# Kernel optimization log

Measured on AMD Instinct MI355X. Metric: run time of the kernel, lower is better.

The kernel has to match this reference:

```python
import jax, jax.numpy as jnp
import numpy as np

GROUPS = 64; SIDE = 8; STEPS = 8
TAU = 1.0; FLOOR = 1e-4; EPS = 1e-4
MU = 1.0; DT = 0.1; GAMMA = 0.1
FLOW_W = 1.0; LOCAL_W = 0.5; KEEP_RATIO = 0.5


def _with_floor(m):
    n = m.shape[-1]
    mask = 1.0 - jnp.eye(n, dtype=m.dtype)
    return jnp.maximum(m * mask, FLOOR * mask)


def _norm_scores(s):
    mean = s.mean(axis=1, keepdims=True)
    std = jnp.clip(s.std(axis=1, ddof=1, keepdims=True), 1e-6, None)  # torch unbiased std
    return (s - mean) / std


def _router_core(tokens, cls_token, W, grid_h, grid_w):
    B, P, D = tokens.shape
    # group ids from patch grid position (patch_indices defaults to arange)
    pi = jnp.broadcast_to(jnp.arange(P), (B, P))
    row, col = pi // grid_w, pi % grid_w
    gh = -(-grid_h // SIDE); gw = -(-grid_w // SIDE)  # ceil div
    gid = jnp.minimum(row // gh, SIDE - 1) * SIDE + jnp.minimum(col // gw, SIDE - 1)  # [B,P]
    # mean-pool tokens per group (scatter_add + count)
    seg = jax.vmap(lambda t, g: jax.ops.segment_sum(t, g, num_segments=GROUPS))
    grouped = seg(tokens, gid)                                 # [B,G,D]
    counts = seg(jnp.ones((B, P, 1), tokens.dtype), gid)       # [B,G,1]
    grouped = grouped / jnp.maximum(counts, 1.0)
    nodes = jnp.concatenate([cls_token[:, None, :], grouped], axis=1)  # [B,G+1,D]
    # pairwise conductance: project, l2-normalize, squared cdist, exp kernel
    proj = jnp.einsum('bnd,ed->bne', nodes, W)  # Linear (no bias): x @ W.T
    proj = proj / jnp.maximum(jnp.linalg.norm(proj, axis=-1, keepdims=True), 1e-12)
    sq = jnp.sum(proj * proj, axis=-1)
    d2 = jnp.maximum(sq[:, :, None] + sq[:, None, :]
                     - 2.0 * jnp.einsum('bnd,bmd->bnm', proj, proj), 0.0)
    C = _with_floor(jnp.exp(-d2 / TAU))
    C = 0.5 * (C + jnp.swapaxes(C, -1, -2))  # symmetric
    # source: cls node injects, groups drain
    source = jnp.full((B, GROUPS + 1), -1.0 / GROUPS, C.dtype).at[:, 0].set(1.0)
    N = GROUPS + 1
    I = jnp.eye(N, dtype=C.dtype)
    d_list, q_list = [C], []
    for _ in range(STEPS):
        deg = C.sum(-1)
        system = deg[:, :, None] * I - C + EPS * I            # Laplacian + eps*I
        p = jnp.linalg.solve(system, source[..., None])[..., 0]
        flow = C * (p[:, :, None] - p[:, None, :])
        q_list.append(flow)
        r = jnp.abs(flow) ** MU
        r = r / (1.0 + r)
        C = C + DT * (r - GAMMA * C)
        C = _with_floor(jnp.maximum(C, 0.0))
        C = _with_floor(0.5 * (C + jnp.swapaxes(C, -1, -2)))
        d_list.append(C)
    return C, jnp.stack(d_list, 1), jnp.stack(q_list, 1), gid


def setup_inputs() -> dict:
    key = jax.random.key(0)
    k1, k2, k3, k4 = jax.random.split(key, 4)
    B, P, D = 64, 576, 768
    return {
        'tokens': jax.random.normal(k1, (B, P, D), jnp.float32),
        'cls_token': jax.random.normal(k2, (B, D), jnp.float32),
        'W': jax.random.normal(k3, (D, D), jnp.float32) / np.sqrt(D),
        'local_scores': jax.random.normal(k4, (B, P), jnp.float32),
        'grid_h': 24,
        'grid_w': 24,
    }


def reference(tokens, cls_token, W, local_scores, grid_h, grid_w):
    B, P, _ = tokens.shape
    final_d, d_hist, q_hist, gid = _router_core(tokens, cls_token, W, grid_h, grid_w)
    routing = final_d[:, 1:, 1:]
    routing = routing / jnp.clip(routing.sum(-1, keepdims=True), 1e-6, None)
    group_flow = jnp.abs(q_hist[:, -1, 1:, :]).sum(-1)        # [B,G]
    group_scores = jnp.take_along_axis(_norm_scores(group_flow), gid, axis=1)
    token_scores = FLOW_W * group_scores + LOCAL_W * _norm_scores(local_scores)
    keep_count = max(1, int(round(P * KEEP_RATIO)))
    _, topk = jax.lax.top_k(token_scores, keep_count)
    patch_keep_mask = jnp.zeros((B, P), bool).at[jnp.arange(B)[:, None], topk].set(True)
    keep_mask = jnp.concatenate([jnp.ones((B, 1), bool), patch_keep_mask], axis=1)
    delta = d_hist[:, 1:] - d_hist[:, :-1]
    aux_sparse = final_d[:, 1:, 1:].sum(axis=(-1, -2)).mean()
    aux_stable = jnp.abs(delta).sum(axis=(-1, -2, -3)).mean()
    return (keep_mask, patch_keep_mask, gid, group_scores, d_hist, q_hist,
            routing, aux_sparse, aux_stable)
```

## Files before the change

kernel.cpp:

```cpp
#include <hip/hip_runtime.h>
#include <stdint.h>

#define NB 64
#define NP 576
#define ND 768
#define NG 64
#define NN 65
#define NSTEPS 8
#define FLOORV 1.0e-4f
#define EPSV   1.0e-4f
#define DTV    0.1f
#define GAMMAV 0.1f
#define KEEPC  288
#define PITCH2 68

__global__ __launch_bounds__(256) void k_group_means(const float* __restrict__ tokens,
                                                     const float* __restrict__ cls,
                                                     float* __restrict__ nodes,
                                                     const int* __restrict__ ghp,
                                                     const int* __restrict__ gwp) {
    int bx = blockIdx.x;
    int b = bx / NN, n = bx - b * NN;
    int tid = threadIdx.x;
    float* orow = nodes + (size_t)bx * ND;
    if (n == 0) {
        for (int d = tid; d < ND; d += 256) orow[d] = cls[(size_t)b * ND + d];
        return;
    }
    int grid_h = *ghp, grid_w = *gwp;
    int gh = (grid_h + 7) / 8, gw = (grid_w + 7) / 8;
    int g = n - 1, gr = g >> 3, gc = g & 7;
    int r0 = gr * gh, r1 = (gr == 7) ? grid_h : min((gr + 1) * gh, grid_h);
    int c0 = gc * gw, c1 = (gc == 7) ? grid_w : min((gc + 1) * gw, grid_w);
    int cnt = (r1 > r0 && c1 > c0) ? (r1 - r0) * (c1 - c0) : 0;
    float cf = (float)max(cnt, 1);
    const float* tb = tokens + (size_t)b * NP * ND;
    for (int d = tid; d < ND; d += 256) {
        float acc = 0.f;
        for (int r = r0; r < r1; ++r)
            for (int c = c0; c < c1; ++c)
                acc += tb[(size_t)(r * grid_w + c) * ND + d];
        orow[d] = acc / cf;
    }
}

__global__ __launch_bounds__(256) void k_gemm_nt(const float* __restrict__ A,
                                                 const float* __restrict__ Bm,
                                                 float* __restrict__ Cm) {
    __shared__ float As[32][68];
    __shared__ float Bs[32][68];
    int tid = threadIdx.x;
    int m0 = blockIdx.x * 64, n0 = blockIdx.y * 64;
    int tx = tid & 15, ty = tid >> 4;
    float acc[4][4];
#pragma unroll
    for (int i = 0; i < 4; ++i)
#pragma unroll
        for (int j = 0; j < 4; ++j) acc[i][j] = 0.f;
    int lrow = tid >> 3, lq = tid & 7;
    for (int k0 = 0; k0 < ND; k0 += 32) {
#pragma unroll
        for (int l = 0; l < 2; ++l) {
            int row = lrow + l * 32;
            float4 va = *(const float4*)&A[(size_t)(m0 + row) * ND + k0 + lq * 4];
            As[lq * 4 + 0][row] = va.x; As[lq * 4 + 1][row] = va.y;
            As[lq * 4 + 2][row] = va.z; As[lq * 4 + 3][row] = va.w;
            float4 vb = *(const float4*)&Bm[(size_t)(n0 + row) * ND + k0 + lq * 4];
            Bs[lq * 4 + 0][row] = vb.x; Bs[lq * 4 + 1][row] = vb.y;
            Bs[lq * 4 + 2][row] = vb.z; Bs[lq * 4 + 3][row] = vb.w;
        }
        __syncthreads();
#pragma unroll
        for (int kk = 0; kk < 32; ++kk) {
            float4 a4 = *(const float4*)&As[kk][ty * 4];
            float4 b4 = *(const float4*)&Bs[kk][tx * 4];
            float av[4] = {a4.x, a4.y, a4.z, a4.w};
            float bv[4] = {b4.x, b4.y, b4.z, b4.w};
#pragma unroll
            for (int i = 0; i < 4; ++i)
#pragma unroll
                for (int j = 0; j < 4; ++j) acc[i][j] += av[i] * bv[j];
        }
        __syncthreads();
    }
#pragma unroll
    for (int i = 0; i < 4; ++i) {
        float4 o = make_float4(acc[i][0], acc[i][1], acc[i][2], acc[i][3]);
        *(float4*)&Cm[(size_t)(m0 + ty * 4 + i) * ND + n0 + tx * 4] = o;
    }
}

__global__ __launch_bounds__(256) void k_normalize(float* __restrict__ proj, float* __restrict__ sqv) {
    int r = blockIdx.x, tid = threadIdx.x;
    __shared__ double red[8];
    __shared__ float invs;
    float* row = proj + (size_t)r * ND;
    double s = 0.0;
    for (int d = tid; d < ND; d += 256) { double v = (double)row[d]; s += v * v; }
#pragma unroll
    for (int off = 32; off; off >>= 1) s += __shfl_down(s, off, 64);
    int wid = tid >> 6, lane = tid & 63;
    if (lane == 0) red[wid] = s;
    __syncthreads();
    if (tid == 0) invs = (float)(1.0 / fmax(sqrt(red[0] + red[1] + red[2] + red[3]), 1e-12));
    __syncthreads();
    float inv = invs;
    double s2 = 0.0;
    for (int d = tid; d < ND; d += 256) {
        float v = row[d] * inv; row[d] = v; s2 += (double)v * (double)v;
    }
#pragma unroll
    for (int off = 32; off; off >>= 1) s2 += __shfl_down(s2, off, 64);
    __syncthreads();
    if (lane == 0) red[wid] = s2;
    __syncthreads();
    if (tid == 0) sqv[r] = (float)(red[0] + red[1] + red[2] + red[3]);
}

__global__ __launch_bounds__(256) void k_pairwise(const float* __restrict__ proj,
                                                  const float* __restrict__ sqv,
                                                  float* __restrict__ dhist) {
    int b = blockIdx.x, tid = threadIdx.x;
    int tx = tid & 15, ty = tid >> 4;
    __shared__ float Ps[NN][65];
    float acc[5][5];
#pragma unroll
    for (int a = 0; a < 5; ++a)
#pragma unroll
        for (int c = 0; c < 5; ++c) acc[a][c] = 0.f;
    const float* Pb = proj + (size_t)b * NN * ND;
    for (int k0 = 0; k0 < ND; k0 += 64) {
        __syncthreads();
        for (int idx = tid; idx < NN * 64; idx += 256) {
            int i = idx >> 6, kk = idx & 63;
            Ps[i][kk] = Pb[(size_t)i * ND + k0 + kk];
        }
        __syncthreads();
        for (int kk = 0; kk < 64; ++kk) {
            float av[5], bv[5];
#pragma unroll
            for (int a = 0; a < 5; ++a) { int i = ty + 16 * a; av[a] = (i < NN) ? Ps[i][kk] : 0.f; }
#pragma unroll
            for (int c = 0; c < 5; ++c) { int j = tx + 16 * c; bv[c] = (j < NN) ? Ps[j][kk] : 0.f; }
#pragma unroll
            for (int a = 0; a < 5; ++a)
#pragma unroll
                for (int c = 0; c < 5; ++c) acc[a][c] += av[a] * bv[c];
        }
    }
#pragma unroll
    for (int a = 0; a < 5; ++a)
#pragma unroll
        for (int c = 0; c < 5; ++c) {
            int i = ty + 16 * a, j = tx + 16 * c;
            if (i < NN && j < NN) {
                float d2 = fmaxf(sqv[b * NN + i] + sqv[b * NN + j] - 2.0f * acc[a][c], 0.f);
                double cv = exp(-(double)d2);
                float cf = (i == j) ? 0.f : fmaxf((float)cv, FLOORV);
                dhist[(size_t)b * 9 * NN * NN + (size_t)i * NN + j] = cf;
            }
        }
}

__global__ __launch_bounds__(256) void k_dynamics(float* __restrict__ dhist,
                                                  float* __restrict__ qhist,
                                                  double* __restrict__ part) {
    int b = blockIdx.x, tid = threadIdx.x;
    __shared__ float Cs[NN * NN];
    __shared__ float Aug[NN * PITCH2];
    __shared__ float pd[NN];
    __shared__ double redd[8];
    float* C0 = dhist + (size_t)b * 9 * NN * NN;
    for (int t = tid; t < NN * NN; t += 256) Cs[t] = C0[t];
    __syncthreads();

    int r = tid >> 2, q = tid & 3;
    const int my_i = r + 1;
    float* mrow = Aug + my_i * PITCH2;
    double stable = 0.0, sparse = 0.0;

#pragma unroll 1
    for (int step = 0; step < NSTEPS; ++step) {
        for (int t = tid; t < NN * PITCH2; t += 256) {
            int i = t / PITCH2, j = t - i * PITCH2;
            if (j != i && j != NN)
                Aug[t] = (j < NN) ? -Cs[i * NN + j] : 0.f;
        }
        if (tid < NN) {
            float s = 0.f;
            const float* cr = Cs + tid * NN;
#pragma unroll 4
            for (int j = 0; j < NN; ++j) s += cr[j];
            Aug[tid * PITCH2 + tid] = s + EPSV;
            Aug[tid * PITCH2 + NN] = (tid == 0) ? 1.0f : (-1.0f / NG);
        }
        __syncthreads();

#pragma unroll 1
        for (int k = 0; k < NN - 1; k += 2) {
            if (my_i > k + 1) {
                const float* P = Aug + k * PITCH2;
                const float* Q = P + PITCH2;
                float Pk = P[k], Pk1 = P[k + 1];
                float Qk = Q[k], Qk1 = Q[k + 1];
                float Aik = mrow[k], Aik1 = mrow[k + 1];
                float invP = 1.0f / Pk;
                float h = Qk * invP;
                float Qd = Qk1 - h * Pk1;
                float f = Aik * invP;
                float g = (Aik1 - f * Pk1) / Qd;
                float c1 = f - g * h, c2 = g;
                const float4* P4 = (const float4*)P;
                const float4* Q4 = (const float4*)Q;
                float4* M4 = (float4*)mrow;
#pragma unroll
                for (int u = 0; u < 4; ++u) {
                    int t = q + 4 * u;
                    float4 p = P4[t], qv = Q4[t], m = M4[t];
                    m.x -= c1 * p.x + c2 * qv.x;
                    m.y -= c1 * p.y + c2 * qv.y;
                    m.z -= c1 * p.z + c2 * qv.z;
                    m.w -= c1 * p.w + c2 * qv.w;
                    M4[t] = m;
                }
                if (q == 0) {
                    float4 p = P4[16], qv = Q4[16], m = M4[16];
                    m.x -= c1 * p.x + c2 * qv.x;
                    m.y -= c1 * p.y + c2 * qv.y;
                    m.z -= c1 * p.z + c2 * qv.z;
                    m.w -= c1 * p.w + c2 * qv.w;
                    M4[16] = m;
                }
            }
            __syncthreads();
        }

        {
            int fr = 2 * (tid >> 3) + 1;
            int l8 = tid & 7;
            float* R = Aug + fr * PITCH2;
            const float* Pp = R - PITCH2;
            float h = R[fr - 1] / Pp[fr - 1];
            float4* R4 = (float4*)R;
            const float4* Pp4 = (const float4*)Pp;
#pragma unroll
            for (int u = 0; u < 2; ++u) {
                int t = l8 + 8 * u;
                float4 a = R4[t], p = Pp4[t];
                a.x -= h * p.x; a.y -= h * p.y; a.z -= h * p.z; a.w -= h * p.w;
                R4[t] = a;
            }
            if (l8 == 0) {
                float4 a = R4[16], p = Pp4[16];
                a.x -= h * p.x; a.y -= h * p.y; a.z -= h * p.z; a.w -= h * p.w;
                R4[16] = a;
            }
        }
        __syncthreads();

        if (tid < 64) {
            int lane = tid;
            int i_own = lane + 1;
            const float* brow = Aug + i_own * PITCH2;
            float inv_own = 1.0f / brow[i_own];
            float rhs = brow[NN];
            float acc = 0.f, p_own = 0.f;
#pragma unroll 2
            for (int i = NN - 1; i >= 1; --i) {
                float t = (rhs - acc) * inv_own;
                float pi = __shfl(t, i - 1, 64);
                if (i_own == i) p_own = t;
                acc += ((lane < i - 1) ? brow[i] : 0.f) * pi;
                if (lane == 0) pd[i] = pi;
            }
            float sp0 = Cs[i_own] * p_own;
#pragma unroll
            for (int off = 32; off; off >>= 1) sp0 += __shfl_down(sp0, off, 64);
            if (lane == 0) pd[0] = (1.0f + sp0) / Aug[0];
        }
        __syncthreads();

        float* qout = qhist + ((size_t)b * NSTEPS + step) * NN * NN;
        float* dout = dhist + ((size_t)b * 9 + step + 1) * NN * NN;
        for (int t = tid; t < NN * NN; t += 256) {
            int i = t / NN, j = t - i * NN;
            float c = Cs[t];
            float fl = c * (pd[i] - pd[j]);
            qout[t] = fl;
            float rr = fabsf(fl); rr = rr / (1.0f + rr);
            float cn = c + DTV * (rr - GAMMAV * c);
            float cnf = (i == j) ? 0.0f : fmaxf(cn, FLOORV);
            Cs[t] = cnf;
            dout[t] = cnf;
            stable += fabs((double)cnf - (double)c);
            if (step == NSTEPS - 1 && i > 0 && j > 0) sparse += (double)cnf;
        }
        __syncthreads();
    }

#pragma unroll
    for (int off = 32; off; off >>= 1) {
        stable += __shfl_down(stable, off, 64);
        sparse += __shfl_down(sparse, off, 64);
    }
    int wid = tid >> 6, lane = tid & 63;
    if (lane == 0) { redd[wid] = stable; redd[4 + wid] = sparse; }
    __syncthreads();
    if (tid == 0) {
        part[b]      = redd[4] + redd[5] + redd[6] + redd[7];
        part[NB + b] = redd[0] + redd[1] + redd[2] + redd[3];
    }
}

__global__ __launch_bounds__(256) void k_scores(const float* __restrict__ qhist,
                                                const float* __restrict__ local,
                                                const int* __restrict__ ghp,
                                                const int* __restrict__ gwp,
                                                float* __restrict__ keep,
                                                float* __restrict__ patch,
                                                float* __restrict__ gidout,
                                                float* __restrict__ gsout) {
    int b = blockIdx.x, tid = threadIdx.x;
    __shared__ double gf[NG];
    __shared__ double ts[NP];
    __shared__ double red[8];
    __shared__ double stats[2];
    if (tid < NG) {
        const float* qrow = qhist + ((size_t)b * NSTEPS + (NSTEPS - 1)) * NN * NN + (size_t)(tid + 1) * NN;
        double s = 0.0;
        for (int j = 0; j < NN; ++j) s += fabs((double)qrow[j]);
        gf[tid] = s;
    }
    __syncthreads();
    if (tid < 64) {
        double v = gf[tid];
        double s = v;
#pragma unroll
        for (int off = 32; off; off >>= 1) s += __shfl_down(s, off, 64);
        double mean = __shfl(s, 0, 64) / (double)NG;
        double d = v - mean, ss = d * d;
#pragma unroll
        for (int off = 32; off; off >>= 1) ss += __shfl_down(ss, off, 64);
        if (tid == 0) { stats[0] = mean; stats[1] = 1.0 / fmax(sqrt(ss / (NG - 1)), 1e-6); }
    }
    const float* lrow = local + (size_t)b * NP;
    double s1 = 0.0;
    for (int p = tid; p < NP; p += 256) s1 += (double)lrow[p];
#pragma unroll
    for (int off = 32; off; off >>= 1) s1 += __shfl_down(s1, off, 64);
    int wid = tid >> 6, lane = tid & 63;
    if (lane == 0) red[wid] = s1;
    __syncthreads();
    double lmean = (red[0] + red[1] + red[2] + red[3]) / (double)NP;
    double s2 = 0.0;
    for (int p = tid; p < NP; p += 256) { double d = (double)lrow[p] - lmean; s2 += d * d; }
#pragma unroll
    for (int off = 32; off; off >>= 1) s2 += __shfl_down(s2, off, 64);
    __syncthreads();
    if (lane == 0) red[wid] = s2;
    __syncthreads();
    double linv = 1.0 / fmax(sqrt((red[0] + red[1] + red[2] + red[3]) / (double)(NP - 1)), 1e-6);
    double gmean = stats[0], ginv = stats[1];
    int grid_h = *ghp, grid_w = *gwp;
    int gh = (grid_h + 7) / 8, gw = (grid_w + 7) / 8;
    for (int p = tid; p < NP; p += 256) {
        int row = p / grid_w, col = p - row * grid_w;
        int g = min(row / gh, 7) * 8 + min(col / gw, 7);
        double gsc = (gf[g] - gmean) * ginv;
        double lsc = ((double)lrow[p] - lmean) * linv;
        ts[p] = gsc + 0.5 * lsc;
        gidout[(size_t)b * NP + p] = (float)g;
        gsout[(size_t)b * NP + p]  = (float)gsc;
    }
    __syncthreads();
    for (int p = tid; p < NP; p += 256) {
        double sp = ts[p];
        int c = 0;
        for (int qq = 0; qq < NP; ++qq) {
            double v = ts[qq];
            c += (v > sp) || (v == sp && qq < p);
        }
        float kf = (c < KEEPC) ? 1.0f : 0.0f;
        patch[(size_t)b * NP + p] = kf;
        keep[(size_t)b * (NP + 1) + 1 + p] = kf;
    }
    if (tid == 0) keep[(size_t)b * (NP + 1)] = 1.0f;
}

__global__ void k_routing(const float* __restrict__ dhist, float* __restrict__ rout) {
    int b = blockIdx.x, tid = threadIdx.x;
    const float* Crow = dhist + ((size_t)b * 9 + 8) * NN * NN + (size_t)(tid + 1) * NN + 1;
    double s = 0.0;
    for (int j = 0; j < NG; ++j) s += (double)Crow[j];
    double inv = 1.0 / fmax(s, 1e-6);
    float* orow = rout + ((size_t)b * NG + tid) * NG;
    for (int j = 0; j < NG; ++j) orow[j] = (float)((double)Crow[j] * inv);
}

__global__ void k_aux(const double* __restrict__ part, float* __restrict__ osp, float* __restrict__ ost) {
    int tid = threadIdx.x;
    double sp = part[tid], st = part[NB + tid];
#pragma unroll
    for (int off = 32; off; off >>= 1) {
        sp += __shfl_down(sp, off, 64);
        st += __shfl_down(st, off, 64);
    }
    if (tid == 0) { *osp = (float)(sp / NB); *ost = (float)(st / NB); }
}

extern "C" void kernel_launch(void* const* d_in, const int* in_sizes, int n_in,
                              void* d_out, int out_size, void* d_ws, size_t ws_size,
                              hipStream_t stream) {
    const float* tokens = (const float*)d_in[0];
    const float* cls    = (const float*)d_in[1];
    const float* W      = (const float*)d_in[2];
    const float* local  = (const float*)d_in[3];
    const int* ghp = (const int*)d_in[4];
    const int* gwp = (const int*)d_in[5];

    float* out = (float*)d_out;
    float* o_keep  = out;
    float* o_patch = o_keep + (size_t)NB * (NP + 1);
    float* o_gid   = o_patch + (size_t)NB * NP;
    float* o_gs    = o_gid + (size_t)NB * NP;
    float* o_dh    = o_gs + (size_t)NB * NP;
    float* o_qh    = o_dh + (size_t)NB * 9 * NN * NN;
    float* o_rt    = o_qh + (size_t)NB * NSTEPS * NN * NN;
    float* o_sp    = o_rt + (size_t)NB * NG * NG;
    float* o_st    = o_sp + 1;

    float* nodes = (float*)d_ws;
    float* proj  = nodes + (size_t)NB * NN * ND;
    float* sqv   = proj + (size_t)NB * NN * ND;
    double* part = (double*)(((uintptr_t)(sqv + NB * NN) + 15) & ~(uintptr_t)15);

    k_group_means<<<NB * NN, 256, 0, stream>>>(tokens, cls, nodes, ghp, gwp);
    dim3 g2((NB * NN) / 64, ND / 64);
    k_gemm_nt<<<g2, 256, 0, stream>>>(nodes, W, proj);
    k_normalize<<<NB * NN, 256, 0, stream>>>(proj, sqv);
    k_pairwise<<<NB, 256, 0, stream>>>(proj, sqv, o_dh);
    k_dynamics<<<NB, 256, 0, stream>>>(o_dh, o_qh, part);
    k_scores<<<NB, 256, 0, stream>>>(o_qh, local, ghp, gwp, o_keep, o_patch, o_gid, o_gs);
    k_routing<<<NB, 64, 0, stream>>>(o_dh, o_rt);
    k_aux<<<1, 64, 0, stream>>>(part, o_sp, o_st);
}
```

Baseline: 719.2 us.

## Use 4-row blocked elimination in Laplacian solve to halve barriers

The Gaussian elimination over the 65x65 augmented system now eliminates four pivot rows per pass instead of two. Each pass inverts the 4x4 pivot block in registers and applies a rank-4 update to every trailing row. This halves the number of block-wide __syncthreads across the 8 solve steps. The in-block cleanup now runs as three barrier-separated sub-steps per 4-row group. The cost is redundant 4x4 inverse work in every thread, more register pressure, and no pivoting within the block, which may change numerical behaviour.

Result: faster. 685.0 us (-4.8%).

```diff
diff --git a/kernel.cpp b/kernel.cpp
--- a/kernel.cpp
+++ b/kernel.cpp
@@ -197,64 +197,94 @@
         __syncthreads();
 
 #pragma unroll 1
-        for (int k = 0; k < NN - 1; k += 2) {
-            if (my_i > k + 1) {
-                const float* P = Aug + k * PITCH2;
-                const float* Q = P + PITCH2;
-                float Pk = P[k], Pk1 = P[k + 1];
-                float Qk = Q[k], Qk1 = Q[k + 1];
-                float Aik = mrow[k], Aik1 = mrow[k + 1];
-                float invP = 1.0f / Pk;
-                float h = Qk * invP;
-                float Qd = Qk1 - h * Pk1;
-                float f = Aik * invP;
-                float g = (Aik1 - f * Pk1) / Qd;
-                float c1 = f - g * h, c2 = g;
-                const float4* P4 = (const float4*)P;
-                const float4* Q4 = (const float4*)Q;
+        for (int k = 0; k < NN - 1; k += 4) {
+            float N4[4][4], Iv[4][4];
+#pragma unroll
+            for (int a = 0; a < 4; ++a)
+#pragma unroll
+                for (int c = 0; c < 4; ++c) {
+                    N4[c][a] = Aug[(k + a) * PITCH2 + k + c];
+                    Iv[c][a] = (a == c) ? 1.0f : 0.0f;
+                }
+#pragma unroll
+            for (int p = 0; p < 4; ++p) {
+                float ip = 1.0f / N4[p][p];
+#pragma unroll
+                for (int c = 0; c < 4; ++c) { N4[p][c] *= ip; Iv[p][c] *= ip; }
+#pragma unroll
+                for (int rr = 0; rr < 4; ++rr) {
+                    if (rr != p) {
+                        float f = N4[rr][p];
+#pragma unroll
+                        for (int c = 0; c < 4; ++c) {
+                            N4[rr][c] -= f * N4[p][c];
+                            Iv[rr][c] -= f * Iv[p][c];
+                        }
+                    }
+                }
+            }
+            if (my_i >= k + 4) {
+                float4 av = *(const float4*)(mrow + k);
+                float x0 = Iv[0][0]*av.x + Iv[0][1]*av.y + Iv[0][2]*av.z + Iv[0][3]*av.w;
+                float x1 = Iv[1][0]*av.x + Iv[1][1]*av.y + Iv[1][2]*av.z + Iv[1][3]*av.w;
+                float x2 = Iv[2][0]*av.x + Iv[2][1]*av.y + Iv[2][2]*av.z + Iv[2][3]*av.w;
+                float x3 = Iv[3][0]*av.x + Iv[3][1]*av.y + Iv[3][2]*av.z + Iv[3][3]*av.w;
+                const float4* P0 = (const float4*)(Aug + (k + 0) * PITCH2);
+                const float4* P1 = (const float4*)(Aug + (k + 1) * PITCH2);
+                const float4* P2 = (const float4*)(Aug + (k + 2) * PITCH2);
+                const float4* P3 = (const float4*)(Aug + (k + 3) * PITCH2);
                 float4* M4 = (float4*)mrow;
 #pragma unroll
-                for (int u = 0; u < 4; ++u) {
+                for (int u = 0; u < 5; ++u) {
                     int t = q + 4 * u;
-                    float4 p = P4[t], qv = Q4[t], m = M4[t];
-                    m.x -= c1 * p.x + c2 * qv.x;
-                    m.y -= c1 * p.y + c2 * qv.y;
-                    m.z -= c1 * p.z + c2 * qv.z;
-                    m.w -= c1 * p.w + c2 * qv.w;
-                    M4[t] = m;
-                }
-                if (q == 0) {
-                    float4 p = P4[16], qv = Q4[16], m = M4[16];
-                    m.x -= c1 * p.x + c2 * qv.x;
-                    m.y -= c1 * p.y + c2 * qv.y;
-                    m.z -= c1 * p.z + c2 * qv.z;
-                    m.w -= c1 * p.w + c2 * qv.w;
-                    M4[16] = m;
+                    if (t < 17) {
+                        float4 m = M4[t];
+                        float4 p0 = P0[t], p1 = P1[t], p2 = P2[t], p3 = P3[t];
+                        m.x -= x0 * p0.x + x1 * p1.x + x2 * p2.x + x3 * p3.x;
+                        m.y -= x0 * p0.y + x1 * p1.y + x2 * p2.y + x3 * p3.y;
+                        m.z -= x0 * p0.z + x1 * p1.z + x2 * p2.z + x3 * p3.z;
+                        m.w -= x0 * p0.w + x1 * p1.w + x2 * p2.w + x3 * p3.w;
+                        M4[t] = m;
+                    }
                 }
             }
             __syncthreads();
         }
 
         {
-            int fr = 2 * (tid >> 3) + 1;
-            int l8 = tid & 7;
-            float* R = Aug + fr * PITCH2;
-            const float* Pp = R - PITCH2;
-            float h = R[fr - 1] / Pp[fr - 1];
-            float4* R4 = (float4*)R;
-            const float4* Pp4 = (const float4*)Pp;
-#pragma unroll
-            for (int u = 0; u < 2; ++u) {
-                int t = l8 + 8 * u;
-                float4 a = R4[t], p = Pp4[t];
-                a.x -= h * p.x; a.y -= h * p.y; a.z -= h * p.z; a.w -= h * p.w;
-                R4[t] = a;
-            }
-            if (l8 == 0) {
-                float4 a = R4[16], p = Pp4[16];
-                a.x -= h * p.x; a.y -= h * p.y; a.z -= h * p.z; a.w -= h * p.w;
-                R4[16] = a;
-            }
+            int g = tid >> 4, l16 = tid & 15;
+            int base = g << 2;
+            float* R0 = Aug + base * PITCH2;
+            float* R1 = R0 + PITCH2;
+            float* R2 = R1 + PITCH2;
+            float* R3 = R2 + PITCH2;
+            float4* R1v = (float4*)R1; float4* R2v = (float4*)R2; float4* R3v = (float4*)R3;
+            const float4* R0v = (const float4*)R0;
+            float inv0 = 1.0f / R0[base];
+            float l10 = R1[base] * inv0;
+            { float4 a = R1v[l16], p = R0v[l16];
+              a.x -= l10*p.x; a.y -= l10*p.y; a.z -= l10*p.z; a.w -= l10*p.w; R1v[l16] = a; }
+            if (l16 == 0) { float4 a = R1v[16], p = R0v[16];
+              a.x -= l10*p.x; a.y -= l10*p.y; a.z -= l10*p.z; a.w -= l10*p.w; R1v[16] = a; }
+            __syncthreads();
+            float l20 = R2[base] * inv0;
+            float l21 = (R2[base+1] - l20 * R0[base+1]) / R1[base+1];
+            { float4 a = R2v[l16], p = R0v[l16], t1 = R1v[l16];
+              a.x -= l20*p.x + l21*t1.x; a.y -= l20*p.y + l21*t1.y;
+              a.z -= l20*p.z + l21*t1.z; a.w -= l20*p.w + l21*t1.w; R2v[l16] = a; }
+            if (l16 == 0) { float4 a = R2v[16], p = R0v[16], t1 = R1v[16];
+              a.x -= l20*p.x + l21*t1.x; a.y -= l20*p.y + l21*t1.y;
+              a.z -= l20*p.z + l21*t1.z; a.w -= l20*p.w + l21*t1.w; R2v[16] = a; }
+            __syncthreads();
+            float l30 = R3[base] * inv0;
+            float l31 = (R3[base+1] - l30 * R0[base+1]) / R1[base+1];
+            float l32 = (R3[base+2] - l30 * R0[base+2] - l31 * R1[base+2]) / R2[base+2];
+            { float4 a = R3v[l16], p = R0v[l16], t1 = R1v[l16], t2 = R2v[l16];
+              a.x -= l30*p.x + l31*t1.x + l32*t2.x; a.y -= l30*p.y + l31*t1.y + l32*t2.y;
+              a.z -= l30*p.z + l31*t1.z + l32*t2.z; a.w -= l30*p.w + l31*t1.w + l32*t2.w; R3v[l16] = a; }
+            if (l16 == 0) { float4 a = R3v[16], p = R0v[16], t1 = R1v[16], t2 = R2v[16];
+              a.x -= l30*p.x + l31*t1.x + l32*t2.x; a.y -= l30*p.y + l31*t1.y + l32*t2.y;
+              a.z -= l30*p.z + l31*t1.z + l32*t2.z; a.w -= l30*p.w + l31*t1.w + l32*t2.w; R3v[16] = a; }
         }
         __syncthreads();
 
```
